# Kernel tuning notes

Measured on AMD Instinct MI355X. Metric: run time of the kernel, lower is better.

## Reference

```python
import jax, jax.numpy as jnp
import numpy as np

N = 100000
E = 600000
H = 128  # embedding_size
DEPTH = 6


def setup_inputs() -> dict:
    key = jax.random.key(0)
    ks = jax.random.split(key, 12)
    X = jax.random.normal(ks[0], (N, 3), dtype=jnp.float32)
    edge_index = jax.random.randint(ks[1], (2, E), 0, N, dtype=jnp.int64)
    s = 1.0 / np.sqrt(H)
    W0 = jax.random.uniform(ks[2], (H, 3), jnp.float32, -s, s)
    b0 = jax.random.uniform(ks[3], (H,), jnp.float32, -s, s)
    W_ih = jax.random.uniform(ks[4], (3 * H, H), jnp.float32, -s, s)
    W_hh = jax.random.uniform(ks[5], (3 * H, H), jnp.float32, -s, s)
    b_ih = jax.random.uniform(ks[6], (3 * H,), jnp.float32, -s, s)
    b_hh = jax.random.uniform(ks[7], (3 * H,), jnp.float32, -s, s)
    Wm1 = jax.random.uniform(ks[8], (H // 2, H), jnp.float32, -s, s)
    bm1 = jax.random.uniform(ks[9], (H // 2,), jnp.float32, -s, s)
    Wm2 = jax.random.uniform(ks[10], (1, H // 2), jnp.float32, -s, s)
    bm2 = jax.random.uniform(ks[11], (1,), jnp.float32, -s, s)
    return {"X": X, "edge_index": edge_index, "W0": W0, "b0": b0,
            "W_ih": W_ih, "W_hh": W_hh, "b_ih": b_ih, "b_hh": b_hh,
            "Wm1": Wm1, "bm1": bm1, "Wm2": Wm2, "bm2": bm2}


def _gcn_agg(h, row, col, norm):
    # out[i] = sum_{e: col[e]==i} norm[e] * h[row[e]]
    msgs = norm[:, None] * h[row]          # [E, H]
    return jax.ops.segment_sum(msgs, col, num_segments=N)


def _gru_cell(x, h, W_ih, W_hh, b_ih, b_hh):
    gx = x @ W_ih.T + b_ih                 # [N, 3H]
    gh = h @ W_hh.T + b_hh                 # [N, 3H]
    xr, xz, xn = jnp.split(gx, 3, axis=1)
    hr, hz, hn = jnp.split(gh, 3, axis=1)
    r = jax.nn.sigmoid(xr + hr)
    z = jax.nn.sigmoid(xz + hz)
    n = jnp.tanh(xn + r * hn)
    return (1.0 - z) * n + z * h


def reference(X, edge_index, W0, b0, W_ih, W_hh, b_ih, b_hh, Wm1, bm1, Wm2, bm2):
    row, col = edge_index[0], edge_index[1]
    # degree over concat(row, col), +1, inv-sqrt with inf->0
    ones = jnp.ones((2 * E,), dtype=X.dtype)
    deg = jax.ops.segment_sum(ones, jnp.concatenate([row, col]), num_segments=N) + 1.0
    deg_inv_sqrt = deg ** -0.5
    deg_inv_sqrt = jnp.where(jnp.isinf(deg_inv_sqrt), 0.0, deg_inv_sqrt)
    norm = deg_inv_sqrt[row] * deg_inv_sqrt[col]  # [E]

    h = jax.nn.leaky_relu(X @ W0.T + b0, negative_slope=0.01)  # [N, H]
    h_max = jnp.full_like(h, -jnp.inf)
    for _ in range(DEPTH - 1):
        h_aggre = _gcn_agg(h, row, col, norm)
        h = _gru_cell(h_aggre, h, W_ih, W_hh, b_ih, b_hh)
        h_max = jnp.maximum(h_max, h)

    hid = jax.nn.leaky_relu(h_max @ Wm1.T + bm1, negative_slope=0.01)
    out = hid @ Wm2.T + bm2                # [N, 1]
    return jnp.squeeze(out, axis=-1)       # [N]
```

## Files before the change

### kernel.cpp

```cpp
#include <hip/hip_runtime.h>

#define Nn 100000
#define Ee 600000
#define Hh 128
#define NP 100096
#define NT (NP / 64)

typedef float f32x4 __attribute__((ext_vector_type(4)));
typedef _Float16 f16x8 __attribute__((ext_vector_type(8)));

static __device__ __forceinline__ float sigmoidf_(float x) {
  return 1.0f / (1.0f + __expf(-x));
}
static __device__ __forceinline__ float tanh_fast(float x) {
  return 1.0f - 2.0f / (__expf(2.0f * x) + 1.0f);
}
static __device__ __forceinline__ int swz(int u) {
  return u ^ (((u >> 11) & 3) << 4);
}

__global__ void count_kernel(const int* __restrict__ ei, int* __restrict__ degi,
                             int* __restrict__ cnt) {
  int e = blockIdx.x * 256 + threadIdx.x;
  if (e >= Ee) return;
  int r = ei[e], c = ei[Ee + e];
  atomicAdd(&degi[r], 1);
  atomicAdd(&degi[c], 1);
  atomicAdd(&cnt[c], 1);
}

__global__ void scan_partial(const int* __restrict__ cnt, const int* __restrict__ degi,
                             float* __restrict__ dis, int* __restrict__ bsum) {
  __shared__ int s[256];
  int i = blockIdx.x * 256 + threadIdx.x;
  s[threadIdx.x] = (i < Nn) ? cnt[i] : 0;
  if (i < Nn) dis[i] = rsqrtf((float)degi[i] + 1.0f);
  __syncthreads();
  for (int off = 128; off > 0; off >>= 1) {
    if (threadIdx.x < off) s[threadIdx.x] += s[threadIdx.x + off];
    __syncthreads();
  }
  if (threadIdx.x == 0) bsum[blockIdx.x] = s[0];
}

__global__ void scan_bsums(const int* __restrict__ bsum, int* __restrict__ bpre, int nb) {
  __shared__ int s[512];
  int t = threadIdx.x;
  s[t] = (t < nb) ? bsum[t] : 0;
  __syncthreads();
  for (int off = 1; off < 512; off <<= 1) {
    int u = (t >= off) ? s[t - off] : 0;
    __syncthreads();
    s[t] += u;
    __syncthreads();
  }
  if (t < nb) bpre[t] = (t == 0) ? 0 : s[t - 1];
}

__global__ void scan_final(const int* __restrict__ cnt, const int* __restrict__ bpre,
                           int* __restrict__ rowptr, int* __restrict__ cursor) {
  __shared__ int s[256];
  int t = threadIdx.x;
  int i = blockIdx.x * 256 + t;
  int v = (i < Nn) ? cnt[i] : 0;
  s[t] = v;
  __syncthreads();
  for (int off = 1; off < 256; off <<= 1) {
    int u = (t >= off) ? s[t - off] : 0;
    __syncthreads();
    s[t] += u;
    __syncthreads();
  }
  int excl = s[t] - v;
  int base = bpre[blockIdx.x];
  if (i < Nn) { rowptr[i] = base + excl; cursor[i] = base + excl; }
  if (i == Nn - 1) rowptr[Nn] = base + excl + v;
}

__global__ void fill_kernel(const int* __restrict__ ei, const float* __restrict__ dis,
                            int* __restrict__ cursor, int* __restrict__ csr_src,
                            float* __restrict__ csr_w) {
  int e = blockIdx.x * 256 + threadIdx.x;
  if (e >= Ee) return;
  int r = ei[e], c = ei[Ee + e];
  int p = atomicAdd(&cursor[c], 1);
  csr_src[p] = r;
  csr_w[p] = dis[r] * dis[c];
}

__global__ void pack_kernel(const float* __restrict__ Wih, const float* __restrict__ Whh,
                            _Float16* __restrict__ Bhi, _Float16* __restrict__ Blo) {
  int t = blockIdx.x * 256 + threadIdx.x;
  if (t >= 8 * 24 * 4 * 16) return;
  int c16 = t & 15;
  int g = (t >> 4) & 3;
  int fid = (t >> 6) % 24;
  int kc = t / (24 * 64);
  int gate = fid >> 3, f = fid & 7;
  int c = f * 16 + c16;
  int wrow = gate * 128 + c;
  size_t base = (size_t)t * 8;
#pragma unroll
  for (int j = 0; j < 8; ++j) {
    int k = kc * 32 + g * 8 + j;
    float v = (k < 128) ? Wih[wrow * 128 + k] : Whh[wrow * 128 + (k - 128)];
    _Float16 hi = (_Float16)v;
    Bhi[base + j] = hi;
    Blo[base + j] = (_Float16)(v - (float)hi);
  }
}

__global__ void pack_mlp(const float* __restrict__ Wm1, _Float16* __restrict__ Bh,
                         _Float16* __restrict__ Bl) {
  int t = blockIdx.x * 256 + threadIdx.x;
  if (t >= 1024) return;
  int c16 = t & 15;
  int g = (t >> 4) & 3;
  int cf = (t >> 6) & 3;
  int kc = t >> 8;
  int c = cf * 16 + c16;
  size_t base = (size_t)t * 8;
#pragma unroll
  for (int j = 0; j < 8; ++j) {
    int k = kc * 32 + g * 8 + j;
    float v = Wm1[c * 128 + k];
    _Float16 hi = (_Float16)v;
    Bh[base + j] = hi;
    Bl[base + j] = (_Float16)(v - (float)hi);
  }
}

__global__ void h0_kernel(const float* __restrict__ X, const float* __restrict__ W0,
                          const float* __restrict__ b0, _Float16* __restrict__ H0) {
  int t = blockIdx.x * 256 + threadIdx.x;
  int i = t >> 7, d = t & 127;
  if (i >= NP) return;
  float v = 0.0f;
  if (i < Nn) {
    float x0 = X[i * 3 + 0], x1 = X[i * 3 + 1], x2 = X[i * 3 + 2];
    v = fmaf(x0, W0[d * 3 + 0], fmaf(x1, W0[d * 3 + 1], fmaf(x2, W0[d * 3 + 2], b0[d])));
    v = v > 0.0f ? v : 0.01f * v;
  }
  H0[(size_t)i * Hh + d] = (_Float16)v;
}

#define DO_GATE_AG(GB, ACC)                                                           \
  {                                                                                   \
    size_t boff = (((size_t)(kc * 24 + (GB)*8 + wave) * 4 + g) * 16 + c16) * 8;       \
    f16x8 bH = *(const f16x8*)(Bhi + boff);                                           \
    f16x8 bL = *(const f16x8*)(Blo + boff);                                           \
    _Pragma("unroll") for (int rf = 0; rf < 4; ++rf)                                  \
        ACC[rf] = __builtin_amdgcn_mfma_f32_16x16x32_f16(aH[rf], bH, ACC[rf], 0, 0, 0); \
    _Pragma("unroll") for (int rf = 0; rf < 4; ++rf)                                  \
        ACC[rf] = __builtin_amdgcn_mfma_f32_16x16x32_f16(aH[rf], bL, ACC[rf], 0, 0, 0); \
    _Pragma("unroll") for (int rf = 0; rf < 4; ++rf)                                  \
        ACC[rf] = __builtin_amdgcn_mfma_f32_16x16x32_f16(aL[rf], bH, ACC[rf], 0, 0, 0); \
  }

#define DO_GATE_H(GB, ACC)                                                            \
  {                                                                                   \
    size_t boff = (((size_t)(kc * 24 + (GB)*8 + wave) * 4 + g) * 16 + c16) * 8;       \
    f16x8 bH = *(const f16x8*)(Bhi + boff);                                           \
    f16x8 bL = *(const f16x8*)(Blo + boff);                                           \
    _Pragma("unroll") for (int rf = 0; rf < 4; ++rf)                                  \
        ACC[rf] = __builtin_amdgcn_mfma_f32_16x16x32_f16(aE[rf], bH, ACC[rf], 0, 0, 0); \
    _Pragma("unroll") for (int rf = 0; rf < 4; ++rf)                                  \
        ACC[rf] = __builtin_amdgcn_mfma_f32_16x16x32_f16(aE[rf], bL, ACC[rf], 0, 0, 0); \
  }

#define GRU_BODY                                                                      \
  const int tid = threadIdx.x;                                                        \
  const int tile = blockIdx.x;                                                        \
  const long rowbase = (long)tile * 64;                                               \
  const int local = tid >> 3;                                                         \
  const int sub = tid & 7;                                                            \
  const int eg = sub & 1;                                                             \
  const int dg = sub >> 1;                                                            \
  const int rf0 = local >> 4, c16l = local & 15;                                      \
  const int lwr = dg * 2048 + rf0 * 512 + c16l * 8;                                   \
  f16x8 own0, own1;                                                                   \
  {                                                                                   \
    const _Float16* p = Hp + (size_t)(rowbase + local) * Hh + dg * 32 + eg * 16;      \
    own0 = *(const f16x8*)p;                                                          \
    own1 = *(const f16x8*)(p + 8);                                                    \
  }                                                                                   \
  {                                                                                   \
    const long node = rowbase + local;                                                \
    float acc[32];                                                                    \
    _Pragma("unroll") for (int m = 0; m < 32; ++m) acc[m] = 0.0f;                     \
    if (node < Nn) {                                                                  \
      const int eEnd = rowptr[node + 1];                                              \
      int e = rowptr[node] + eg;                                                      \
      const _Float16* hb = Hp + dg * 32;                                              \
      for (; e + 2 < eEnd; e += 4) {                                                  \
        const int s0 = csr_src[e], s1 = csr_src[e + 2];                               \
        const float w0 = csr_w[e], w1 = csr_w[e + 2];                                 \
        const f16x8* p0 = (const f16x8*)(hb + (size_t)s0 * Hh);                       \
        const f16x8* p1 = (const f16x8*)(hb + (size_t)s1 * Hh);                       \
        f16x8 va[4], vb[4];                                                           \
        _Pragma("unroll") for (int q = 0; q < 4; ++q) va[q] = p0[q];                  \
        _Pragma("unroll") for (int q = 0; q < 4; ++q) vb[q] = p1[q];                  \
        _Pragma("unroll") for (int q = 0; q < 4; ++q)                                 \
            _Pragma("unroll") for (int m = 0; m < 8; ++m)                             \
                acc[q * 8 + m] = fmaf(w1, (float)vb[q][m],                            \
                                      fmaf(w0, (float)va[q][m], acc[q * 8 + m]));     \
      }                                                                               \
      if (e < eEnd) {                                                                 \
        const int s0 = csr_src[e];                                                    \
        const float w0 = csr_w[e];                                                    \
        const f16x8* p0 = (const f16x8*)(hb + (size_t)s0 * Hh);                       \
        f16x8 va[4];                                                                  \
        _Pragma("unroll") for (int q = 0; q < 4; ++q) va[q] = p0[q];                  \
        _Pragma("unroll") for (int q = 0; q < 4; ++q)                                 \
            _Pragma("unroll") for (int m = 0; m < 8; ++m)                             \
                acc[q * 8 + m] = fmaf(w0, (float)va[q][m], acc[q * 8 + m]);           \
      }                                                                               \
    }                                                                                 \
    _Pragma("unroll") for (int m = 0; m < 32; ++m) acc[m] += __shfl_xor(acc[m], 1);   \
    if (eg == 0) {                                                                    \
      _Pragma("unroll") for (int g2 = 0; g2 < 4; ++g2) {                              \
        f16x8 vh, vl;                                                                 \
        _Pragma("unroll") for (int j = 0; j < 8; ++j) {                               \
          float v = acc[g2 * 8 + j];                                                  \
          _Float16 hi = (_Float16)v;                                                  \
          vh[j] = hi;                                                                 \
          vl[j] = (_Float16)(v - (float)hi);                                          \
        }                                                                             \
        const int o = swz(lwr + g2 * 128);                                            \
        *(f16x8*)(SH + o) = vh;                                                       \
        *(f16x8*)(SL + o) = vl;                                                       \
      }                                                                               \
    }                                                                                 \
    *(f16x8*)(SE + swz(lwr + (eg * 2 + 0) * 128)) = own0;                             \
    *(f16x8*)(SE + swz(lwr + (eg * 2 + 1) * 128)) = own1;                             \
  }                                                                                   \
  __syncthreads();                                                                    \
  const int wave = tid >> 6, lane = tid & 63;                                         \
  const int g = lane >> 4, c16 = lane & 15;                                           \
  const int lbase = g * 128 + c16 * 8;                                                \
  f32x4 accR[4], accZ[4], accXN[4], accHN[4];                                         \
  _Pragma("unroll") for (int rf = 0; rf < 4; ++rf) {                                  \
    accR[rf] = (f32x4){0.f, 0.f, 0.f, 0.f};                                           \
    accZ[rf] = (f32x4){0.f, 0.f, 0.f, 0.f};                                           \
    accXN[rf] = (f32x4){0.f, 0.f, 0.f, 0.f};                                          \
    accHN[rf] = (f32x4){0.f, 0.f, 0.f, 0.f};                                          \
  }                                                                                   \
  _Pragma("unroll") for (int kc = 0; kc < 4; ++kc) {                                  \
    f16x8 aH[4], aL[4];                                                               \
    _Pragma("unroll") for (int rf = 0; rf < 4; ++rf) {                                \
      int off = swz(kc * 2048 + rf * 512 + lbase);                                    \
      aH[rf] = *(const f16x8*)(SH + off);                                             \
      aL[rf] = *(const f16x8*)(SL + off);                                             \
    }                                                                                 \
    DO_GATE_AG(0, accR)                                                               \
    DO_GATE_AG(1, accZ)                                                               \
    DO_GATE_AG(2, accXN)                                                              \
  }                                                                                   \
  _Pragma("unroll") for (int kc = 4; kc < 8; ++kc) {                                  \
    f16x8 aE[4];                                                                      \
    _Pragma("unroll") for (int rf = 0; rf < 4; ++rf) {                                \
      int off = swz((kc - 4) * 2048 + rf * 512 + lbase);                              \
      aE[rf] = *(const f16x8*)(SE + off);                                             \
    }                                                                                 \
    DO_GATE_H(0, accR)                                                                \
    DO_GATE_H(1, accZ)                                                                \
    DO_GATE_H(2, accHN)                                                               \
  }                                                                                   \
  const int c = wave * 16 + c16;                                                      \
  const float br = bih[c] + bhh[c];                                                   \
  const float bz = bih[128 + c] + bhh[128 + c];                                       \
  const float bxn = bih[256 + c];                                                     \
  const float bhn = bhh[256 + c];                                                     \
  const int kcs = c >> 5;                                                             \
  const int gs = (c >> 3) & 3;                                                        \
  const int js = c & 7;

__global__ __launch_bounds__(512, 4) void gcn_gru_fused(
    const _Float16* __restrict__ Hp, _Float16* __restrict__ Hn,
    const int* __restrict__ csr_src, const float* __restrict__ csr_w,
    const int* __restrict__ rowptr,
    const _Float16* __restrict__ Bhi, const _Float16* __restrict__ Blo,
    const float* __restrict__ bih, const float* __restrict__ bhh) {
  __shared__ ushort SH[8192];
  __shared__ ushort SL[8192];
  __shared__ ushort SE[8192];
  GRU_BODY
#pragma unroll
  for (int rf = 0; rf < 4; ++rf) {
#pragma unroll
    for (int reg = 0; reg < 4; ++reg) {
      const int lr = g * 4 + reg;
      const int hoff = swz(kcs * 2048 + rf * 512 + gs * 128 + lr * 8 + js);
      float hold = (float)*(const _Float16*)&SE[hoff];
      float rr = sigmoidf_(accR[rf][reg] + br);
      float zz = sigmoidf_(accZ[rf][reg] + bz);
      float nn = tanh_fast(accXN[rf][reg] + bxn + rr * (accHN[rf][reg] + bhn));
      Hn[(size_t)(rowbase + rf * 16 + lr) * Hh + c] =
          (_Float16)((1.0f - zz) * nn + zz * hold);
    }
  }
}

__global__ __launch_bounds__(512, 4) void gcn_gru_last2(
    const _Float16* __restrict__ Hp, const _Float16* __restrict__ Ha,
    const _Float16* __restrict__ Hb, const _Float16* __restrict__ Hc,
    const int* __restrict__ csr_src, const float* __restrict__ csr_w,
    const int* __restrict__ rowptr,
    const _Float16* __restrict__ Bhi, const _Float16* __restrict__ Blo,
    const float* __restrict__ bih, const float* __restrict__ bhh,
    const _Float16* __restrict__ Bmh, const _Float16* __restrict__ Bml,
    const float* __restrict__ bm1, const float* __restrict__ Wm2,
    const float* __restrict__ bm2, float* __restrict__ out) {
  __shared__ ushort S[16384];
  __shared__ ushort SE[8192];
  ushort* SH = S;
  ushort* SL = S + 8192;
  GRU_BODY
  __syncthreads();
#pragma unroll
  for (int rf = 0; rf < 4; ++rf) {
#pragma unroll
    for (int reg = 0; reg < 4; ++reg) {
      const int lr = g * 4 + reg;
      const int hoff = swz(kcs * 2048 + rf * 512 + gs * 128 + lr * 8 + js);
      float hold = (float)*(const _Float16*)&SE[hoff];
      float rr = sigmoidf_(accR[rf][reg] + br);
      float zz = sigmoidf_(accZ[rf][reg] + bz);
      float nn = tanh_fast(accXN[rf][reg] + bxn + rr * (accHN[rf][reg] + bhn));
      *(_Float16*)&SL[hoff] = (_Float16)((1.0f - zz) * nn + zz * hold);
    }
  }
  __syncthreads();

  {
    const size_t o = (size_t)(rowbase + local) * Hh + dg * 32 + eg * 16;
#pragma unroll
    for (int h2 = 0; h2 < 2; ++h2) {
      const int slot = swz(lwr + (eg * 2 + h2) * 128);
      f16x8 m = *(const f16x8*)(SL + slot);
      f16x8 v;
      v = *(const f16x8*)(Hp + o + h2 * 8);
#pragma unroll
      for (int mm = 0; mm < 8; ++mm) m[mm] = m[mm] > v[mm] ? m[mm] : v[mm];
      v = *(const f16x8*)(Ha + o + h2 * 8);
#pragma unroll
      for (int mm = 0; mm < 8; ++mm) m[mm] = m[mm] > v[mm] ? m[mm] : v[mm];
      v = *(const f16x8*)(Hb + o + h2 * 8);
#pragma unroll
      for (int mm = 0; mm < 8; ++mm) m[mm] = m[mm] > v[mm] ? m[mm] : v[mm];
      v = *(const f16x8*)(Hc + o + h2 * 8);
#pragma unroll
      for (int mm = 0; mm < 8; ++mm) m[mm] = m[mm] > v[mm] ? m[mm] : v[mm];
      *(f16x8*)(SH + slot) = m;
    }
  }
  __syncthreads();

  const int cf = wave >> 1, kh = wave & 1;
  f32x4 macc[4];
#pragma unroll
  for (int rf = 0; rf < 4; ++rf) macc[rf] = (f32x4){0.f, 0.f, 0.f, 0.f};
#pragma unroll
  for (int q = 0; q < 2; ++q) {
    const int kc = kh * 2 + q;
    f16x8 aE[4];
#pragma unroll
    for (int rf = 0; rf < 4; ++rf) {
      int off = swz(kc * 2048 + rf * 512 + lbase);
      aE[rf] = *(const f16x8*)(SH + off);
    }
    size_t boff = (((size_t)(kc * 4 + cf) * 4 + g) * 16 + c16) * 8;
    f16x8 bH = *(const f16x8*)(Bmh + boff);
    f16x8 bL = *(const f16x8*)(Bml + boff);
#pragma unroll
    for (int rf = 0; rf < 4; ++rf)
      macc[rf] = __builtin_amdgcn_mfma_f32_16x16x32_f16(aE[rf], bH, macc[rf], 0, 0, 0);
#pragma unroll
    for (int rf = 0; rf < 4; ++rf)
      macc[rf] = __builtin_amdgcn_mfma_f32_16x16x32_f16(aE[rf], bL, macc[rf], 0, 0, 0);
  }
  __syncthreads();

  float* hid = (float*)S;
  const int hc = cf * 16 + c16;
  if (kh == 0) {
#pragma unroll
    for (int rf = 0; rf < 4; ++rf)
#pragma unroll
      for (int reg = 0; reg < 4; ++reg)
        hid[(rf * 16 + g * 4 + reg) * 66 + hc] = macc[rf][reg];
  }
  __syncthreads();
  if (kh == 1) {
#pragma unroll
    for (int rf = 0; rf < 4; ++rf)
#pragma unroll
      for (int reg = 0; reg < 4; ++reg)
        hid[(rf * 16 + g * 4 + reg) * 66 + hc] += macc[rf][reg];
  }
  __syncthreads();

  {
    const int row = tid >> 3;
    const int s8 = tid & 7;
    float s = 0.f;
#pragma unroll
    for (int j = 0; j < 8; ++j) {
      const int cc = s8 * 8 + j;
      float v = hid[row * 66 + cc] + bm1[cc];
      v = v > 0.f ? v : 0.01f * v;
      s = fmaf(v, Wm2[cc], s);
    }
    s += __shfl_xor(s, 1);
    s += __shfl_xor(s, 2);
    s += __shfl_xor(s, 4);
    if (s8 == 0) {
      long grow = rowbase + row;
      if (grow < Nn) out[grow] = s + bm2[0];
    }
  }
}

extern "C" void kernel_launch(void* const* d_in, const int* in_sizes, int n_in,
                              void* d_out, int out_size, void* d_ws, size_t ws_size,
                              hipStream_t stream) {
  const float* X = (const float*)d_in[0];
  const int* ei = (const int*)d_in[1];
  const float* W0 = (const float*)d_in[2];
  const float* b0 = (const float*)d_in[3];
  const float* Wih = (const float*)d_in[4];
  const float* Whh = (const float*)d_in[5];
  const float* bih = (const float*)d_in[6];
  const float* bhh = (const float*)d_in[7];
  const float* Wm1 = (const float*)d_in[8];
  const float* bm1 = (const float*)d_in[9];
  const float* Wm2 = (const float*)d_in[10];
  const float* bm2 = (const float*)d_in[11];
  float* out = (float*)d_out;

  char* ws = (char*)d_ws;
  size_t off = 0;
  auto alloc = [&](size_t bytes) -> void* {
    void* p = ws + off;
    off = (off + bytes + 255) & ~(size_t)255;
    return p;
  };
  _Float16* Hs[5];
  for (int i = 0; i < 5; ++i) Hs[i] = (_Float16*)alloc((size_t)NP * Hh * 2);
  _Float16* Bhi = (_Float16*)alloc((size_t)8 * 24 * 4 * 16 * 8 * 2);
  _Float16* Blo = (_Float16*)alloc((size_t)8 * 24 * 4 * 16 * 8 * 2);
  _Float16* Bmh = (_Float16*)alloc((size_t)1024 * 8 * 2);
  _Float16* Bml = (_Float16*)alloc((size_t)1024 * 8 * 2);
  float* dis = (float*)alloc((size_t)Nn * 4);
  int* degi = (int*)alloc((size_t)Nn * 4);
  int* cnt = (int*)alloc((size_t)Nn * 4);
  int* rowptr = (int*)alloc((size_t)(Nn + 1) * 4);
  int* cursor = (int*)alloc((size_t)Nn * 4);
  int* bsum = (int*)alloc(512 * 4);
  int* bpre = (int*)alloc(512 * 4);
  int* csr_src = (int*)alloc((size_t)Ee * 4);
  float* csr_w = (float*)alloc((size_t)Ee * 4);
  (void)ws_size;
  (void)in_sizes;
  (void)n_in;
  (void)out_size;

  const int NB = (Nn + 255) / 256;
  const int EB = (Ee + 255) / 256;

  hipMemsetAsync(degi, 0, (size_t)Nn * 4, stream);
  hipMemsetAsync(cnt, 0, (size_t)Nn * 4, stream);
  count_kernel<<<EB, 256, 0, stream>>>(ei, degi, cnt);
  scan_partial<<<NB, 256, 0, stream>>>(cnt, degi, dis, bsum);
  scan_bsums<<<1, 512, 0, stream>>>(bsum, bpre, NB);
  scan_final<<<NB, 256, 0, stream>>>(cnt, bpre, rowptr, cursor);
  fill_kernel<<<EB, 256, 0, stream>>>(ei, dis, cursor, csr_src, csr_w);
  pack_kernel<<<48, 256, 0, stream>>>(Wih, Whh, Bhi, Blo);
  pack_mlp<<<4, 256, 0, stream>>>(Wm1, Bmh, Bml);
  h0_kernel<<<(NP * Hh) / 256, 256, 0, stream>>>(X, W0, b0, Hs[0]);

  for (int t = 1; t <= 4; ++t) {
    gcn_gru_fused<<<NT, 512, 0, stream>>>(Hs[t - 1], Hs[t], csr_src, csr_w,
                                          rowptr, Bhi, Blo, bih, bhh);
  }
  gcn_gru_last2<<<NT, 512, 0, stream>>>(Hs[4], Hs[1], Hs[2], Hs[3], csr_src, csr_w,
                                        rowptr, Bhi, Blo, bih, bhh, Bmh, Bml,
                                        bm1, Wm2, bm2, out);
}
```

Measured before the change: 570.2 us.

## Drop split-fp16 aggregate operand, pack degree counters, merge prep kernels

The aggregated message in the GRU input GEMM is now stored as a single fp16 value instead of a hi/lo split pair. This removes one third of the input-gate MFMAs and halves the shared-memory staging for that operand. The degree and in-count atomics are packed into one 64-bit atomic per endpoint, which drops one atomic and one memset. The weight packing and h0 kernels are merged into one launch. The cost is lower precision in the aggregate-times-W_ih product, which could increase numerical error against the fp32 reference.

Result: faster. 519.9 us (-8.8%).

```diff
diff --git a/kernel.cpp b/kernel.cpp
--- a/kernel.cpp
+++ b/kernel.cpp
@@ -19,22 +19,22 @@
   return u ^ (((u >> 11) & 3) << 4);
 }
 
-__global__ void count_kernel(const int* __restrict__ ei, int* __restrict__ degi,
-                             int* __restrict__ cnt) {
+__global__ void count_kernel(const int* __restrict__ ei,
+                             unsigned long long* __restrict__ pk) {
   int e = blockIdx.x * 256 + threadIdx.x;
   if (e >= Ee) return;
   int r = ei[e], c = ei[Ee + e];
-  atomicAdd(&degi[r], 1);
-  atomicAdd(&degi[c], 1);
-  atomicAdd(&cnt[c], 1);
-}
-
-__global__ void scan_partial(const int* __restrict__ cnt, const int* __restrict__ degi,
+  atomicAdd(&pk[r], 1ULL << 32);
+  atomicAdd(&pk[c], (1ULL << 32) | 1ULL);
+}
+
+__global__ void scan_partial(const unsigned long long* __restrict__ pk,
                              float* __restrict__ dis, int* __restrict__ bsum) {
   __shared__ int s[256];
   int i = blockIdx.x * 256 + threadIdx.x;
-  s[threadIdx.x] = (i < Nn) ? cnt[i] : 0;
-  if (i < Nn) dis[i] = rsqrtf((float)degi[i] + 1.0f);
+  unsigned long long p = (i < Nn) ? pk[i] : 0ULL;
+  s[threadIdx.x] = (int)(unsigned)p;
+  if (i < Nn) dis[i] = rsqrtf((float)(unsigned)(p >> 32) + 1.0f);
   __syncthreads();
   for (int off = 128; off > 0; off >>= 1) {
     if (threadIdx.x < off) s[threadIdx.x] += s[threadIdx.x + off];
@@ -57,12 +57,13 @@
   if (t < nb) bpre[t] = (t == 0) ? 0 : s[t - 1];
 }
 
-__global__ void scan_final(const int* __restrict__ cnt, const int* __restrict__ bpre,
+__global__ void scan_final(const unsigned long long* __restrict__ pk,
+                           const int* __restrict__ bpre,
                            int* __restrict__ rowptr, int* __restrict__ cursor) {
   __shared__ int s[256];
   int t = threadIdx.x;
   int i = blockIdx.x * 256 + t;
-  int v = (i < Nn) ? cnt[i] : 0;
+  int v = (i < Nn) ? (int)(unsigned)pk[i] : 0;
   s[t] = v;
   __syncthreads();
   for (int off = 1; off < 256; off <<= 1) {
@@ -88,76 +89,63 @@
   csr_w[p] = dis[r] * dis[c];
 }
 
-__global__ void pack_kernel(const float* __restrict__ Wih, const float* __restrict__ Whh,
-                            _Float16* __restrict__ Bhi, _Float16* __restrict__ Blo) {
-  int t = blockIdx.x * 256 + threadIdx.x;
-  if (t >= 8 * 24 * 4 * 16) return;
-  int c16 = t & 15;
-  int g = (t >> 4) & 3;
-  int fid = (t >> 6) % 24;
-  int kc = t / (24 * 64);
-  int gate = fid >> 3, f = fid & 7;
-  int c = f * 16 + c16;
-  int wrow = gate * 128 + c;
-  size_t base = (size_t)t * 8;
-#pragma unroll
-  for (int j = 0; j < 8; ++j) {
-    int k = kc * 32 + g * 8 + j;
-    float v = (k < 128) ? Wih[wrow * 128 + k] : Whh[wrow * 128 + (k - 128)];
-    _Float16 hi = (_Float16)v;
-    Bhi[base + j] = hi;
-    Blo[base + j] = (_Float16)(v - (float)hi);
-  }
-}
-
-__global__ void pack_mlp(const float* __restrict__ Wm1, _Float16* __restrict__ Bh,
-                         _Float16* __restrict__ Bl) {
-  int t = blockIdx.x * 256 + threadIdx.x;
-  if (t >= 1024) return;
-  int c16 = t & 15;
-  int g = (t >> 4) & 3;
-  int cf = (t >> 6) & 3;
-  int kc = t >> 8;
-  int c = cf * 16 + c16;
-  size_t base = (size_t)t * 8;
-#pragma unroll
-  for (int j = 0; j < 8; ++j) {
-    int k = kc * 32 + g * 8 + j;
-    float v = Wm1[c * 128 + k];
-    _Float16 hi = (_Float16)v;
-    Bh[base + j] = hi;
-    Bl[base + j] = (_Float16)(v - (float)hi);
-  }
-}
-
-__global__ void h0_kernel(const float* __restrict__ X, const float* __restrict__ W0,
+__global__ void prep_misc(const float* __restrict__ Wih, const float* __restrict__ Whh,
+                          _Float16* __restrict__ Bhi, _Float16* __restrict__ Blo,
+                          const float* __restrict__ Wm1, _Float16* __restrict__ Bmh,
+                          _Float16* __restrict__ Bml,
+                          const float* __restrict__ X, const float* __restrict__ W0,
                           const float* __restrict__ b0, _Float16* __restrict__ H0) {
-  int t = blockIdx.x * 256 + threadIdx.x;
-  int i = t >> 7, d = t & 127;
-  if (i >= NP) return;
-  float v = 0.0f;
-  if (i < Nn) {
-    float x0 = X[i * 3 + 0], x1 = X[i * 3 + 1], x2 = X[i * 3 + 2];
-    v = fmaf(x0, W0[d * 3 + 0], fmaf(x1, W0[d * 3 + 1], fmaf(x2, W0[d * 3 + 2], b0[d])));
-    v = v > 0.0f ? v : 0.01f * v;
-  }
-  H0[(size_t)i * Hh + d] = (_Float16)v;
-}
-
-#define DO_GATE_AG(GB, ACC)                                                           \
-  {                                                                                   \
-    size_t boff = (((size_t)(kc * 24 + (GB)*8 + wave) * 4 + g) * 16 + c16) * 8;       \
-    f16x8 bH = *(const f16x8*)(Bhi + boff);                                           \
-    f16x8 bL = *(const f16x8*)(Blo + boff);                                           \
-    _Pragma("unroll") for (int rf = 0; rf < 4; ++rf)                                  \
-        ACC[rf] = __builtin_amdgcn_mfma_f32_16x16x32_f16(aH[rf], bH, ACC[rf], 0, 0, 0); \
-    _Pragma("unroll") for (int rf = 0; rf < 4; ++rf)                                  \
-        ACC[rf] = __builtin_amdgcn_mfma_f32_16x16x32_f16(aH[rf], bL, ACC[rf], 0, 0, 0); \
-    _Pragma("unroll") for (int rf = 0; rf < 4; ++rf)                                  \
-        ACC[rf] = __builtin_amdgcn_mfma_f32_16x16x32_f16(aL[rf], bH, ACC[rf], 0, 0, 0); \
-  }
-
-#define DO_GATE_H(GB, ACC)                                                            \
+  const int b = blockIdx.x;
+  if (b < 48) {
+    int t = b * 256 + threadIdx.x;
+    int c16 = t & 15;
+    int g = (t >> 4) & 3;
+    int fid = (t >> 6) % 24;
+    int kc = t / (24 * 64);
+    int gate = fid >> 3, f = fid & 7;
+    int c = f * 16 + c16;
+    int wrow = gate * 128 + c;
+    size_t base = (size_t)t * 8;
+#pragma unroll
+    for (int j = 0; j < 8; ++j) {
+      int k = kc * 32 + g * 8 + j;
+      float v = (k < 128) ? Wih[wrow * 128 + k] : Whh[wrow * 128 + (k - 128)];
+      _Float16 hi = (_Float16)v;
+      Bhi[base + j] = hi;
+      Blo[base + j] = (_Float16)(v - (float)hi);
+    }
+  } else if (b < 52) {
+    int t = (b - 48) * 256 + threadIdx.x;
+    int c16 = t & 15;
+    int g = (t >> 4) & 3;
+    int cf = (t >> 6) & 3;
+    int kc = t >> 8;
+    int c = cf * 16 + c16;
+    size_t base = (size_t)t * 8;
+#pragma unroll
+    for (int j = 0; j < 8; ++j) {
+      int k = kc * 32 + g * 8 + j;
+      float v = Wm1[c * 128 + k];
+      _Float16 hi = (_Float16)v;
+      Bmh[base + j] = hi;
+      Bml[base + j] = (_Float16)(v - (float)hi);
+    }
+  } else {
+    int t = (b - 52) * 256 + threadIdx.x;
+    int i = t >> 7, d = t & 127;
+    if (i >= NP) return;
+    float v = 0.0f;
+    if (i < Nn) {
+      float x0 = X[i * 3 + 0], x1 = X[i * 3 + 1], x2 = X[i * 3 + 2];
+      v = fmaf(x0, W0[d * 3 + 0],
+               fmaf(x1, W0[d * 3 + 1], fmaf(x2, W0[d * 3 + 2], b0[d])));
+      v = v > 0.0f ? v : 0.01f * v;
+    }
+    H0[(size_t)i * Hh + d] = (_Float16)v;
+  }
+}
+
+#define DO_GATE(GB, ACC)                                                              \
   {                                                                                   \
     size_t boff = (((size_t)(kc * 24 + (GB)*8 + wave) * 4 + g) * 16 + c16) * 8;       \
     f16x8 bH = *(const f16x8*)(Bhi + boff);                                           \
@@ -219,16 +207,10 @@
     _Pragma("unroll") for (int m = 0; m < 32; ++m) acc[m] += __shfl_xor(acc[m], 1);   \
     if (eg == 0) {                                                                    \
       _Pragma("unroll") for (int g2 = 0; g2 < 4; ++g2) {                              \
-        f16x8 vh, vl;                                                                 \
-        _Pragma("unroll") for (int j = 0; j < 8; ++j) {                               \
-          float v = acc[g2 * 8 + j];                                                  \
-          _Float16 hi = (_Float16)v;                                                  \
-          vh[j] = hi;                                                                 \
-          vl[j] = (_Float16)(v - (float)hi);                                          \
-        }                                                                             \
-        const int o = swz(lwr + g2 * 128);                                            \
-        *(f16x8*)(SH + o) = vh;                                                       \
-        *(f16x8*)(SL + o) = vl;                                                       \
+        f16x8 vh;                                                                     \
+        _Pragma("unroll") for (int j = 0; j < 8; ++j)                                 \
+            vh[j] = (_Float16)acc[g2 * 8 + j];                                        \
+        *(f16x8*)(SA + swz(lwr + g2 * 128)) = vh;                                     \
       }                                                                               \
     }                                                                                 \
     *(f16x8*)(SE + swz(lwr + (eg * 2 + 0) * 128)) = own0;                             \
@@ -246,15 +228,14 @@
     accHN[rf] = (f32x4){0.f, 0.f, 0.f, 0.f};                                          \
   }                                                                                   \
   _Pragma("unroll") for (int kc = 0; kc < 4; ++kc) {                                  \
-    f16x8 aH[4], aL[4];                                                               \
+    f16x8 aE[4];                                                                      \
     _Pragma("unroll") for (int rf = 0; rf < 4; ++rf) {                                \
       int off = swz(kc * 2048 + rf * 512 + lbase);                                    \
-      aH[rf] = *(const f16x8*)(SH + off);                                             \
-      aL[rf] = *(const f16x8*)(SL + off);                                             \
+      aE[rf] = *(const f16x8*)(SA + off);                                             \
     }                                                                                 \
-    DO_GATE_AG(0, accR)                                                               \
-    DO_GATE_AG(1, accZ)                                                               \
-    DO_GATE_AG(2, accXN)                                                              \
+    DO_GATE(0, accR)                                                                  \
+    DO_GATE(1, accZ)                                                                  \
+    DO_GATE(2, accXN)                                                                 \
   }                                                                                   \
   _Pragma("unroll") for (int kc = 4; kc < 8; ++kc) {                                  \
     f16x8 aE[4];                                                                      \
@@ -262,9 +243,9 @@
       int off = swz((kc - 4) * 2048 + rf * 512 + lbase);                              \
       aE[rf] = *(const f16x8*)(SE + off);                                             \
     }                                                                                 \
-    DO_GATE_H(0, accR)                                                                \
-    DO_GATE_H(1, accZ)                                                                \
-    DO_GATE_H(2, accHN)                                                               \
+    DO_GATE(0, accR)                                                                  \
+    DO_GATE(1, accZ)                                                                  \
+    DO_GATE(2, accHN)                                                                 \
   }                                                                                   \
   const int c = wave * 16 + c16;                                                      \
   const float br = bih[c] + bhh[c];                                                   \
@@ -281,8 +262,7 @@
     const int* __restrict__ rowptr,
     const _Float16* __restrict__ Bhi, const _Float16* __restrict__ Blo,
     const float* __restrict__ bih, const float* __restrict__ bhh) {
-  __shared__ ushort SH[8192];
-  __shared__ ushort SL[8192];
+  __shared__ ushort SA[8192];
   __shared__ ushort SE[8192];
   GRU_BODY
 #pragma unroll
@@ -312,9 +292,8 @@
     const float* __restrict__ bm1, const float* __restrict__ Wm2,
     const float* __restrict__ bm2, float* __restrict__ out) {
   __shared__ ushort S[16384];
-  __shared__ ushort SE[8192];
-  ushort* SH = S;
-  ushort* SL = S + 8192;
+  ushort* SA = S;
+  ushort* SE = S + 8192;
   GRU_BODY
   __syncthreads();
 #pragma unroll
@@ -327,7 +306,7 @@
       float rr = sigmoidf_(accR[rf][reg] + br);
       float zz = sigmoidf_(accZ[rf][reg] + bz);
       float nn = tanh_fast(accXN[rf][reg] + bxn + rr * (accHN[rf][reg] + bhn));
-      *(_Float16*)&SL[hoff] = (_Float16)((1.0f - zz) * nn + zz * hold);
+      *(_Float16*)&SA[hoff] = (_Float16)((1.0f - zz) * nn + zz * hold);
     }
   }
   __syncthreads();
@@ -337,7 +316,7 @@
 #pragma unroll
     for (int h2 = 0; h2 < 2; ++h2) {
       const int slot = swz(lwr + (eg * 2 + h2) * 128);
-      f16x8 m = *(const f16x8*)(SL + slot);
+      f16x8 m = *(const f16x8*)(SA + slot);
       f16x8 v;
       v = *(const f16x8*)(Hp + o + h2 * 8);
 #pragma unroll
@@ -351,7 +330,7 @@
       v = *(const f16x8*)(Hc + o + h2 * 8);
 #pragma unroll
       for (int mm = 0; mm < 8; ++mm) m[mm] = m[mm] > v[mm] ? m[mm] : v[mm];
-      *(f16x8*)(SH + slot) = m;
+      *(f16x8*)(SA + slot) = m;
     }
   }
   __syncthreads();
@@ -367,7 +346,7 @@
 #pragma unroll
     for (int rf = 0; rf < 4; ++rf) {
       int off = swz(kc * 2048 + rf * 512 + lbase);
-      aE[rf] = *(const f16x8*)(SH + off);
+      aE[rf] = *(const f16x8*)(SA + off);
     }
     size_t boff = (((size_t)(kc * 4 + cf) * 4 + g) * 16 + c16) * 8;
     f16x8 bH = *(const f16x8*)(Bmh + boff);
@@ -452,8 +431,7 @@
   _Float16* Bmh = (_Float16*)alloc((size_t)1024 * 8 * 2);
   _Float16* Bml = (_Float16*)alloc((size_t)1024 * 8 * 2);
   float* dis = (float*)alloc((size_t)Nn * 4);
-  int* degi = (int*)alloc((size_t)Nn * 4);
-  int* cnt = (int*)alloc((size_t)Nn * 4);
+  unsigned long long* pk = (unsigned long long*)alloc((size_t)Nn * 8);
   int* rowptr = (int*)alloc((size_t)(Nn + 1) * 4);
   int* cursor = (int*)alloc((size_t)Nn * 4);
   int* bsum = (int*)alloc(512 * 4);
@@ -468,16 +446,14 @@
   const int NB = (Nn + 255) / 256;
   const int EB = (Ee + 255) / 256;
 
-  hipMemsetAsync(degi, 0, (size_t)Nn * 4, stream);
-  hipMemsetAsync(cnt, 0, (size_t)Nn * 4, stream);
-  count_kernel<<<EB, 256, 0, stream>>>(ei, degi, cnt);
-  scan_partial<<<NB, 256, 0, stream>>>(cnt, degi, dis, bsum);
+  hipMemsetAsync(pk, 0, (size_t)Nn * 8, stream);
+  count_kernel<<<EB, 256, 0, stream>>>(ei, pk);
+  scan_partial<<<NB, 256, 0, stream>>>(pk, dis, bsum);
   scan_bsums<<<1, 512, 0, stream>>>(bsum, bpre, NB);
-  scan_final<<<NB, 256, 0, stream>>>(cnt, bpre, rowptr, cursor);
+  scan_final<<<NB, 256, 0, stream>>>(pk, bpre, rowptr, cursor);
   fill_kernel<<<EB, 256, 0, stream>>>(ei, dis, cursor, csr_src, csr_w);
-  pack_kernel<<<48, 256, 0, stream>>>(Wih, Whh, Bhi, Blo);
-  pack_mlp<<<4, 256, 0, stream>>>(Wm1, Bmh, Bml);
-  h0_kernel<<<(NP * Hh) / 256, 256, 0, stream>>>(X, W0, b0, Hs[0]);
+  prep_misc<<<52 + (NP * Hh) / 256, 256, 0, stream>>>(Wih, Whh, Bhi, Blo, Wm1, Bmh,
+                                                      Bml, X, W0, b0, Hs[0]);
 
   for (int t = 1; t <= 4; ++t) {
     gcn_gru_fused<<<NT, 512, 0, stream>>>(Hs[t - 1], Hs[t], csr_src, csr_w,
```
